# Optimization experiments

Hardware: AMD Instinct MI355X
Metric: run time of the kernel (lower is better)

The kernel has to match this reference:

```python
import jax, jax.numpy as jnp
import numpy as np

RES, RES_, STRIDE = 28, 14, 2
H, KD, AR = 8, 16, 4
SCALE = KD ** -0.5
EPS = 1e-5


def make_bias_idxs(res=RES, res_=RES_, stride=STRIDE):
    pts = [(i, j) for i in range(res) for j in range(res)]
    pts_ = [(i, j) for i in range(res_) for j in range(res_)]
    offs, idxs = {}, []
    for p1 in pts_:
        for p2 in pts:
            off = (abs(p1[0] * stride - p2[0]), abs(p1[1] * stride - p2[1]))
            if off not in offs:
                offs[off] = len(offs)
            idxs.append(offs[off])
    return np.array(idxs, dtype=np.int32).reshape(len(pts_), len(pts)), len(offs)


def setup_inputs() -> dict:
    key = jax.random.key(0)
    ks = jax.random.split(key, 16)
    idxs, n_off = make_bias_idxs()  # n_off == 784
    B, N, C = 128, RES * RES, 256
    d_kv, d_q, d_p, d_pin = 640, 128, 384, 512
    return {
        "hidden_state": jax.random.normal(ks[0], (B, N, C), jnp.float32),
        "w_kv": jax.random.normal(ks[1], (d_kv, C), jnp.float32) * 0.05,
        "kv_gamma": jax.random.uniform(ks[2], (d_kv,), jnp.float32, 0.5, 1.5),
        "kv_beta": jax.random.normal(ks[3], (d_kv,), jnp.float32) * 0.1,
        "kv_mean": jax.random.normal(ks[4], (d_kv,), jnp.float32) * 0.1,
        "kv_var": jax.random.uniform(ks[5], (d_kv,), jnp.float32, 0.5, 1.5),
        "w_q": jax.random.normal(ks[6], (d_q, C), jnp.float32) * 0.05,
        "q_gamma": jax.random.uniform(ks[7], (d_q,), jnp.float32, 0.5, 1.5),
        "q_beta": jax.random.normal(ks[8], (d_q,), jnp.float32) * 0.1,
        "q_mean": jax.random.normal(ks[9], (d_q,), jnp.float32) * 0.1,
        "q_var": jax.random.uniform(ks[10], (d_q,), jnp.float32, 0.5, 1.5),
        "w_proj": jax.random.normal(ks[11], (d_p, d_pin), jnp.float32) * 0.05,
        "p_gamma": jax.random.uniform(ks[12], (d_p,), jnp.float32, 0.5, 1.5),
        "p_beta": jax.random.normal(ks[13], (d_p,), jnp.float32) * 0.1,
        "p_mean": jax.random.normal(ks[14], (d_p,), jnp.float32) * 0.1,
        "p_var": jax.random.uniform(ks[15], (d_p,), jnp.float32, 0.5, 1.5),
        "attention_biases": jax.random.normal(jax.random.fold_in(key, 99), (H, n_off), jnp.float32),
        "attention_bias_idxs": jnp.asarray(idxs),
    }


def _bn(x, gamma, beta, mean, var):
    # eval-mode BatchNorm1d over last dim
    return (x - mean) * (gamma * jax.lax.rsqrt(var + EPS)) + beta


def _hardswish(x):
    return x * jnp.clip(x + 3.0, 0.0, 6.0) * (1.0 / 6.0)


def reference(hidden_state, w_kv, kv_gamma, kv_beta, kv_mean, kv_var,
              w_q, q_gamma, q_beta, q_mean, q_var,
              w_proj, p_gamma, p_beta, p_mean, p_var,
              attention_biases, attention_bias_idxs):
    B, N, C = hidden_state.shape
    N_ = RES_ * RES_
    # kv: [B, N, 640] -> key [B,H,N,KD], value [B,H,N,AR*KD]
    kv = _bn(hidden_state @ w_kv.T, kv_gamma, kv_beta, kv_mean, kv_var)
    kv = kv.reshape(B, N, H, KD + AR * KD)
    k = jnp.transpose(kv[..., :KD], (0, 2, 1, 3))          # [B,H,N,KD]
    v = jnp.transpose(kv[..., KD:], (0, 2, 1, 3))          # [B,H,N,AR*KD]
    # strided query subsample on the spatial grid
    hs = hidden_state.reshape(B, RES, RES, C)[:, ::STRIDE, ::STRIDE].reshape(B, N_, C)
    q = _bn(hs @ w_q.T, q_gamma, q_beta, q_mean, q_var)
    q = jnp.transpose(q.reshape(B, N_, H, KD), (0, 2, 1, 3))  # [B,H,N_,KD]
    bias = attention_biases[:, attention_bias_idxs]           # [H,N_,N] gathered
    attn = jnp.einsum('bhqd,bhkd->bhqk', q, k) * SCALE + bias
    attn = jax.nn.softmax(attn, axis=-1)
    out = jnp.einsum('bhqk,bhkd->bhqd', attn, v)              # [B,H,N_,AR*KD]
    out = jnp.transpose(out, (0, 2, 1, 3)).reshape(B, N_, H * AR * KD)
    out = _bn(_hardswish(out) @ w_proj.T, p_gamma, p_beta, p_mean, p_var)
    return out
```

## Files before the change

### kernel.cpp

```cpp
#include <hip/hip_runtime.h>

typedef _Float16 f16;
typedef __attribute__((ext_vector_type(2))) _Float16 f16x2;
typedef __attribute__((ext_vector_type(4))) _Float16 f16x4;
typedef __attribute__((ext_vector_type(8))) _Float16 f16x8;
typedef __attribute__((ext_vector_type(4))) float fvec4;
typedef __attribute__((ext_vector_type(4))) float f32x4;
typedef __attribute__((ext_vector_type(16))) float f32x16;
typedef __attribute__((ext_vector_type(4))) unsigned int uint4v;

#define NKEY 784
#define NKEYP 800
#define NQ 196
#define NQP 224

static __device__ __forceinline__ f32x4 mfma16(f16x8 a, f16x8 b, f32x4 c) {
    return __builtin_amdgcn_mfma_f32_16x16x32_f16(a, b, c, 0, 0, 0);
}
static __device__ __forceinline__ f32x16 mfma32(f16x8 a, f16x8 b, f32x16 c) {
    return __builtin_amdgcn_mfma_f32_32x32x16_f16(a, b, c, 0, 0, 0);
}
static __device__ __forceinline__ unsigned pk2(float a, float b) {
    f16x2 t; t[0] = (_Float16)a; t[1] = (_Float16)b;
    return __builtin_bit_cast(unsigned, t);
}
static __device__ __forceinline__ f32x16 z16() {
    f32x16 v;
#pragma unroll
    for (int i = 0; i < 16; ++i) v[i] = 0.f;
    return v;
}

__global__ void prep_scales_all(const float* __restrict__ kg, const float* __restrict__ kb,
                                const float* __restrict__ km, const float* __restrict__ kvv,
                                const float* __restrict__ qg, const float* __restrict__ qb,
                                const float* __restrict__ qm, const float* __restrict__ qv,
                                const float* __restrict__ pg, const float* __restrict__ pb,
                                const float* __restrict__ pm, const float* __restrict__ pv,
                                float* __restrict__ sb) {
    int i = blockIdx.x * 256 + threadIdx.x;
    if (i < 640) {
        float s = kg[i] * rsqrtf(kvv[i] + 1e-5f);
        sb[i] = s; sb[640 + i] = kb[i] - km[i] * s;
    } else if (i < 768) {
        int j = i - 640;
        float s = qg[j] * rsqrtf(qv[j] + 1e-5f);
        sb[1280 + j] = s; sb[1408 + j] = qb[j] - qm[j] * s;
    } else if (i < 1152) {
        int j = i - 768;
        float s = pg[j] * rsqrtf(pv[j] + 1e-5f);
        sb[1536 + j] = s; sb[1920 + j] = pb[j] - pm[j] * s;
    }
}

__global__ void conv_w(const float* __restrict__ wkv, const float* __restrict__ wq,
                       const float* __restrict__ wp, f16* __restrict__ out) {
    int i = blockIdx.x * 256 + threadIdx.x;
    const float* src;
    f16* dst;
    int kc, n, K;
    if (i < 20480)      { int j = i;         kc = j / 640, n = j - kc * 640; src = wkv; dst = out + (size_t)j * 8;            K = 256; }
    else if (i < 24576) { int j = i - 20480; kc = j / 128, n = j - kc * 128; src = wq;  dst = out + 163840 + (size_t)j * 8;   K = 256; }
    else                { int j = i - 24576; kc = j / 384, n = j - kc * 384; src = wp;  dst = out + 196608 + (size_t)j * 8;   K = 512; }
    const float* s = src + (size_t)n * K + kc * 8;
    fvec4 v0 = *(const fvec4*)s;
    fvec4 v1 = *(const fvec4*)(s + 4);
    f16x8 h;
    h[0] = (f16)v0[0]; h[1] = (f16)v0[1]; h[2] = (f16)v0[2]; h[3] = (f16)v0[3];
    h[4] = (f16)v1[0]; h[5] = (f16)v1[1]; h[6] = (f16)v1[2]; h[7] = (f16)v1[3];
    *(f16x8*)dst = h;
}

__global__ void prep_bias(const float* __restrict__ biases, const int* __restrict__ idxs,
                          f16* __restrict__ biasT, int n_off) {
    int tid = blockIdx.x * 256 + threadIdx.x;
    int h = tid / (NQP * NKEYP);
    int rem = tid - h * (NQP * NKEYP);
    int q = rem / NKEYP;
    int key = rem - q * NKEYP;
    float v = 0.f;
    if (q < NQ && key < NKEY) v = biases[h * n_off + idxs[q * NKEY + key]];
    biasT[tid] = (f16)v;
}

template <int MODE>
__global__ __launch_bounds__(256) void gemm_db(
        const void* __restrict__ Ap, const f16x8* __restrict__ Wg,
        const float* __restrict__ sc, const float* __restrict__ sh,
        void* __restrict__ OutA, f16* __restrict__ OutV) {
    constexpr int K     = (MODE == 2) ? 512 : 256;
    constexpr int KS    = K / 32;
    constexpr int CHUNK = (MODE == 2) ? 16 : 32;
    constexpr int NFR   = CHUNK / 16;
    constexpr int NT    = (MODE == 0) ? 640 : (MODE == 1 ? 128 : 384);
    constexpr int NCH   = (MODE == 0) ? 10 : (MODE == 1 ? 4 : 12);
    constexpr int UNITS = (K / 8) * CHUNK;
    constexpr int SR    = UNITS / 256;

    __shared__ f16x8 Wl[2][UNITS];

    const int t = threadIdx.x;
    const int lane = t & 63, wid = t >> 6;
    const int fr = lane & 15, kg = lane >> 4;
    const int m0 = blockIdx.x * 64;
    const int nb0 = blockIdx.y * (NCH * CHUNK);
    const int mrow = m0 + wid * 16 + fr;

    size_t arow;
    if constexpr (MODE == 1) {
        int b = mrow / 196, nn = mrow - b * 196;
        arow = (size_t)b * 784 + (nn / 14) * 56 + (nn % 14) * 2;
    } else {
        arow = (size_t)mrow;
    }
    f16x8 af[KS];
#pragma unroll
    for (int ks = 0; ks < KS; ++ks) {
        if constexpr (MODE == 2) {
            af[ks] = *(const f16x8*)((const f16*)Ap + arow * K + ks * 32 + kg * 8);
        } else {
            const float* a = (const float*)Ap + arow * 256 + ks * 32 + kg * 8;
            fvec4 v0 = *(const fvec4*)a;
            fvec4 v1 = *(const fvec4*)(a + 4);
            f16x8 hv;
            hv[0] = (f16)v0[0]; hv[1] = (f16)v0[1]; hv[2] = (f16)v0[2]; hv[3] = (f16)v0[3];
            hv[4] = (f16)v1[0]; hv[5] = (f16)v1[1]; hv[6] = (f16)v1[2]; hv[7] = (f16)v1[3];
            af[ks] = hv;
        }
    }

#pragma unroll
    for (int rr = 0; rr < SR; ++rr) {
        const int idx = rr * 256 + t;
        Wl[0][idx] = Wg[(size_t)(idx / CHUNK) * NT + nb0 + (idx % CHUNK)];
    }
    __syncthreads();

    const int rg = kg * 4;
    int cur = 0;
    for (int c = 0; c < NCH; ++c) {
        const int n0c = nb0 + c * CHUNK;

        f16x8 nx0, nx1, nx2, nx3;
        if (c + 1 < NCH) {
            const int n0n = n0c + CHUNK;
            nx0 = Wg[(size_t)((0 * 256 + t) / CHUNK) * NT + n0n + ((0 * 256 + t) % CHUNK)];
            nx1 = Wg[(size_t)((1 * 256 + t) / CHUNK) * NT + n0n + ((1 * 256 + t) % CHUNK)];
            nx2 = Wg[(size_t)((2 * 256 + t) / CHUNK) * NT + n0n + ((2 * 256 + t) % CHUNK)];
            nx3 = Wg[(size_t)((3 * 256 + t) / CHUNK) * NT + n0n + ((3 * 256 + t) % CHUNK)];
        }

        f32x4 acc[NFR];
#pragma unroll
        for (int j = 0; j < NFR; ++j) acc[j] = (f32x4){0.f, 0.f, 0.f, 0.f};
#pragma unroll
        for (int ks = 0; ks < KS; ++ks) {
            f16x8 bfr[NFR];
#pragma unroll
            for (int nf = 0; nf < NFR; ++nf)
                bfr[nf] = Wl[cur][(ks * 4 + kg) * CHUNK + nf * 16 + fr];
#pragma unroll
            for (int nf = 0; nf < NFR; ++nf)
                acc[nf] = mfma16(af[ks], bfr[nf], acc[nf]);
        }

        const int mbase = m0 + wid * 16 + rg;
#pragma unroll
        for (int nf = 0; nf < NFR; ++nf) {
            const int n = n0c + nf * 16 + fr;
            const float scn = sc[n], shn = sh[n];
            if constexpr (MODE == 0) {
                const int b = mbase / 784;
                const int nn = mbase - b * 784;
                const int hd = n / 80;
                const int cc = n - hd * 80;
                const size_t bh = (size_t)(b * 8 + hd);
                if (cc < 16) {
#pragma unroll
                    for (int r = 0; r < 4; ++r) {
                        float y = acc[nf][r] * scn + shn;
                        ((f16*)OutA)[(bh * NKEYP + nn + r) * 16 + cc] = (f16)y;
                    }
                } else {
                    const int kbk = nn >> 5, off = nn & 31;
                    f16x4 pv;
#pragma unroll
                    for (int r = 0; r < 4; ++r) pv[r] = (f16)(acc[nf][r] * scn + shn);
                    *(f16x4*)(OutV + ((bh * 25 + kbk) * 64 + (cc - 16)) * 32 + off) = pv;
                }
            } else if constexpr (MODE == 1) {
                const int b = mbase / 196;
                const int nn = mbase - b * 196;
                const int hd = n >> 4, cc = n & 15;
                const size_t bh = (size_t)(b * 8 + hd);
#pragma unroll
                for (int r = 0; r < 4; ++r) {
                    float y = acc[nf][r] * scn + shn;
                    ((f16*)OutA)[(bh * NQP + nn + r) * 16 + cc] = (f16)y;
                }
            } else {
#pragma unroll
                for (int r = 0; r < 4; ++r) {
                    float y = acc[nf][r] * scn + shn;
                    ((float*)OutA)[(size_t)(mbase + r) * 384 + n] = y;
                }
            }
        }

        if (c + 1 < NCH) {
            Wl[cur ^ 1][0 * 256 + t] = nx0;
            Wl[cur ^ 1][1 * 256 + t] = nx1;
            Wl[cur ^ 1][2 * 256 + t] = nx2;
            Wl[cur ^ 1][3 * 256 + t] = nx3;
            __syncthreads();
            cur ^= 1;
        }
    }
}

__global__ __launch_bounds__(448) void attn_fused(const f16* __restrict__ kb,
                                                  const f16* __restrict__ vtb,
                                                  const f16* __restrict__ qw,
                                                  const f16* __restrict__ biasT,
                                                  f16* __restrict__ ao) {
    const int bh = blockIdx.x;
    const int b = bh >> 3, h = bh & 7;
    const int wid = threadIdx.x >> 6;
    const int lane = threadIdx.x & 63;
    const int l31 = lane & 31;
    const int hh = lane >> 5;
    const int q0 = wid * 32;

    const f16* kp = kb + (size_t)bh * (NKEYP * 16);
    const f16* vp = vtb + (size_t)bh * (25 * 64 * 32) + l31 * 32;
    const f16x8 bq = *(const f16x8*)(qw + ((size_t)bh * NQP + q0 + l31) * 16 + hh * 8);
    const f16* bbq = biasT + ((size_t)h * NQP + (q0 + l31)) * NKEYP;

    float mrun = -1e30f;
    float lsum = 0.f;
    f32x16 o0 = z16(), o1 = z16();

    for (int key0 = 0; key0 < NKEY; key0 += 32) {
        f16x8 ak = *(const f16x8*)(kp + (size_t)(key0 + l31) * 16 + hh * 8);
        f32x16 s = mfma32(ak, bq, z16());
        const bool tail = (key0 + 32) > NKEY;
        f16x4 bw[4];
#pragma unroll
        for (int g = 0; g < 4; ++g)
            bw[g] = *(const f16x4*)(bbq + key0 + g * 8 + hh * 4);
        float p[16];
        float cmax = -3.0e38f;
#pragma unroll
        for (int r = 0; r < 16; ++r) {
            const int cr = (r & 3) + ((r >> 2) << 3) + (hh << 2);
            float sv = s[r] * 0.25f + (float)bw[r >> 2][r & 3];
            if (tail && (key0 + cr) >= NKEY) sv = -1e30f;
            p[r] = sv;
            cmax = fmaxf(cmax, sv);
        }
        cmax = fmaxf(cmax, __shfl_xor(cmax, 32));
        if (__any(cmax > mrun + 8.f)) {
            float mnew = fmaxf(mrun, cmax);
            float f = __expf(mrun - mnew);
            mrun = mnew;
            lsum *= f;
#pragma unroll
            for (int r = 0; r < 16; ++r) {
                const int cr = (r & 3) + ((r >> 2) << 3) + (hh << 2);
                float fr2 = __shfl(f, cr);
                o0[r] *= fr2;
                o1[r] *= fr2;
            }
        }
        float psum = 0.f;
#pragma unroll
        for (int r = 0; r < 16; ++r) {
            p[r] = __expf(p[r] - mrun);
            psum += p[r];
        }
        lsum += psum;
        unsigned g0l = pk2(p[0], p[1]),   g0h = pk2(p[2], p[3]);
        unsigned g1l = pk2(p[4], p[5]),   g1h = pk2(p[6], p[7]);
        unsigned g2l = pk2(p[8], p[9]),   g2h = pk2(p[10], p[11]);
        unsigned g3l = pk2(p[12], p[13]), g3h = pk2(p[14], p[15]);
        __builtin_amdgcn_s_setprio(1);
        const f16* vkb = vp + (key0 >> 5) * (64 * 32);
#pragma unroll
        for (int sH = 0; sH < 2; ++sH) {
            unsigned self_lo = sH ? (hh ? g3l : g2l) : (hh ? g1l : g0l);
            unsigned self_hi = sH ? (hh ? g3h : g2h) : (hh ? g1h : g0h);
            unsigned tx_lo   = sH ? (hh ? g2l : g3l) : (hh ? g0l : g1l);
            unsigned tx_hi   = sH ? (hh ? g2h : g3h) : (hh ? g0h : g1h);
            unsigned rx_lo = __shfl_xor(tx_lo, 32);
            unsigned rx_hi = __shfl_xor(tx_hi, 32);
            uint4v w;
            w[0] = hh ? rx_lo : self_lo;
            w[1] = hh ? rx_hi : self_hi;
            w[2] = hh ? self_lo : rx_lo;
            w[3] = hh ? self_hi : rx_hi;
            f16x8 pa = __builtin_bit_cast(f16x8, w);
            const f16* vrow = vkb + sH * 16 + hh * 8;
            f16x8 bv0 = *(const f16x8*)(vrow);
            f16x8 bv1 = *(const f16x8*)(vrow + 32 * 32);
            o0 = mfma32(pa, bv0, o0);
            o1 = mfma32(pa, bv1, o1);
        }
        __builtin_amdgcn_s_setprio(0);
    }
    lsum += __shfl_xor(lsum, 32);
    const float inv = 1.0f / lsum;
#pragma unroll
    for (int r = 0; r < 16; ++r) {
        const int cr = (r & 3) + ((r >> 2) << 3) + (hh << 2);
        const float iq = __shfl(inv, cr);
        const int qg = q0 + cr;
        if (qg < NQ) {
            float v0 = o0[r] * iq, v1 = o1[r] * iq;
            float h0 = v0 * fminf(fmaxf(v0 + 3.f, 0.f), 6.f) * (1.f / 6.f);
            float h1 = v1 * fminf(fmaxf(v1 + 3.f, 0.f), 6.f) * (1.f / 6.f);
            f16* dst = ao + ((size_t)b * NQ + qg) * 512 + h * 64 + l31;
            dst[0] = (f16)h0;
            dst[32] = (f16)h1;
        }
    }
}

extern "C" void kernel_launch(void* const* d_in, const int* in_sizes, int n_in,
                              void* d_out, int out_size, void* d_ws, size_t ws_size,
                              hipStream_t stream) {
    (void)n_in; (void)out_size; (void)ws_size;
    const float* hidden = (const float*)d_in[0];
    const float* w_kv   = (const float*)d_in[1];
    const float* w_q    = (const float*)d_in[6];
    const float* w_p    = (const float*)d_in[11];
    const float* biases = (const float*)d_in[16];
    const int*   idxs   = (const int*)d_in[17];
    const int n_off = in_sizes[16] / 8;

    char* ws = (char*)d_ws;
    const size_t OFF_K  = 0;
    const size_t OFF_V  = 26214400;
    const size_t OFF_Q  = 131072000;
    const size_t OFF_AO = 138412032;
    const size_t OFF_BT = 164102144;
    const size_t OFF_W  = 166969344;
    const size_t OFF_SC = 167755776;
    f16*   kbuf  = (f16*)(ws + OFF_K);
    f16*   vbuf  = (f16*)(ws + OFF_V);
    f16*   qbuf  = (f16*)(ws + OFF_Q);
    f16*   aobuf = (f16*)(ws + OFF_AO);
    f16*   btbuf = (f16*)(ws + OFF_BT);
    f16*   wf16  = (f16*)(ws + OFF_W);
    float* scbuf = (float*)(ws + OFF_SC);

    prep_scales_all<<<5, 256, 0, stream>>>(
        (const float*)d_in[2], (const float*)d_in[3], (const float*)d_in[4], (const float*)d_in[5],
        (const float*)d_in[7], (const float*)d_in[8], (const float*)d_in[9], (const float*)d_in[10],
        (const float*)d_in[12], (const float*)d_in[13], (const float*)d_in[14], (const float*)d_in[15],
        scbuf);
    conv_w<<<192, 256, 0, stream>>>(w_kv, w_q, w_p, wf16);
    prep_bias<<<5600, 256, 0, stream>>>(biases, idxs, btbuf, n_off);
    hipMemsetAsync(qbuf, 0, (size_t)1024 * NQP * 16 * 2, stream);
    gemm_db<0><<<dim3(1568, 2), 256, 0, stream>>>(hidden, (const f16x8*)wf16, scbuf, scbuf + 640, kbuf, vbuf);
    gemm_db<1><<<dim3(392, 1), 256, 0, stream>>>(hidden, (const f16x8*)(wf16 + 163840), scbuf + 1280, scbuf + 1408, qbuf, nullptr);
    attn_fused<<<1024, 448, 0, stream>>>(kbuf, vbuf, qbuf, btbuf, aobuf);
    gemm_db<2><<<dim3(392, 2), 256, 0, stream>>>(aobuf, (const f16x8*)(wf16 + 196608), scbuf + 1536, scbuf + 1920, d_out, nullptr);
}
```

Baseline: 226.6 us.

## Relayout bias and V tiles for coalesced MFMA-fragment loads, use exp2 softmax

The gathered bias table is now written in the exact per-lane MFMA accumulator order, so each lane fetches its 16 bias values with two contiguous 16-byte loads instead of four scattered 8-byte loads. The bias is pre-multiplied by log2(e) so the softmax can use exp2 with a folded scale. The V tile layout is split into 16-key halves so each lane's fragment read is a contiguous 16-byte row chunk. These changes target global-memory load efficiency in the attention inner loop, at the cost of more complex index arithmetic in the prep and GEMM-epilogue kernels.

```diff
diff --git a/kernel.cpp b/kernel.cpp
--- a/kernel.cpp
+++ b/kernel.cpp
@@ -13,6 +13,9 @@
 #define NKEYP 800
 #define NQ 196
 #define NQP 224
+#define LOG2E 1.442695041f
+#define SC2   0.360673760f
+#define THR2  11.5415603f
 
 static __device__ __forceinline__ f32x4 mfma16(f16x8 a, f16x8 b, f32x4 c) {
     return __builtin_amdgcn_mfma_f32_16x16x32_f16(a, b, c, 0, 0, 0);
@@ -72,15 +75,20 @@
 }
 
 __global__ void prep_bias(const float* __restrict__ biases, const int* __restrict__ idxs,
-                          f16* __restrict__ biasT, int n_off) {
+                          f16* __restrict__ biasS, int n_off) {
     int tid = blockIdx.x * 256 + threadIdx.x;
-    int h = tid / (NQP * NKEYP);
-    int rem = tid - h * (NQP * NKEYP);
-    int q = rem / NKEYP;
-    int key = rem - q * NKEYP;
+    const int r = tid & 15;
+    const int lane = (tid >> 4) & 63;
+    const int g = tid >> 10;
+    const int kbk = g % 25;
+    const int tmp = g / 25;
+    const int qt = tmp % 7;
+    const int h = tmp / 7;
+    const int q = qt * 32 + (lane & 31);
+    const int key = kbk * 32 + (r & 3) + 8 * (r >> 2) + 4 * (lane >> 5);
     float v = 0.f;
-    if (q < NQ && key < NKEY) v = biases[h * n_off + idxs[q * NKEY + key]];
-    biasT[tid] = (f16)v;
+    if (q < NQ && key < NKEY) v = biases[h * n_off + idxs[q * NKEY + key]] * LOG2E;
+    biasS[tid] = (f16)v;
 }
 
 template <int MODE>
@@ -182,11 +190,11 @@
                         ((f16*)OutA)[(bh * NKEYP + nn + r) * 16 + cc] = (f16)y;
                     }
                 } else {
-                    const int kbk = nn >> 5, off = nn & 31;
+                    const int kbk = nn >> 5, sH = (nn >> 4) & 1, kk = nn & 15;
                     f16x4 pv;
 #pragma unroll
                     for (int r = 0; r < 4; ++r) pv[r] = (f16)(acc[nf][r] * scn + shn);
-                    *(f16x4*)(OutV + ((bh * 25 + kbk) * 64 + (cc - 16)) * 32 + off) = pv;
+                    *(f16x4*)(OutV + ((bh * 25 + kbk) * 2 + sH) * 1024 + (cc - 16) * 16 + kk) = pv;
                 }
             } else if constexpr (MODE == 1) {
                 const int b = mbase / 196;
@@ -221,7 +229,7 @@
 __global__ __launch_bounds__(448) void attn_fused(const f16* __restrict__ kb,
                                                   const f16* __restrict__ vtb,
                                                   const f16* __restrict__ qw,
-                                                  const f16* __restrict__ biasT,
+                                                  const f16* __restrict__ biasS,
                                                   f16* __restrict__ ao) {
     const int bh = blockIdx.x;
     const int b = bh >> 3, h = bh & 7;
@@ -232,36 +240,36 @@
     const int q0 = wid * 32;
 
     const f16* kp = kb + (size_t)bh * (NKEYP * 16);
-    const f16* vp = vtb + (size_t)bh * (25 * 64 * 32) + l31 * 32;
+    const f16* vp = vtb + (size_t)bh * 51200;
     const f16x8 bq = *(const f16x8*)(qw + ((size_t)bh * NQP + q0 + l31) * 16 + hh * 8);
-    const f16* bbq = biasT + ((size_t)h * NQP + (q0 + l31)) * NKEYP;
+    const f16* bbase = biasS + (((size_t)(h * 7 + wid) * 25) * 64 + lane) * 16;
 
     float mrun = -1e30f;
     float lsum = 0.f;
     f32x16 o0 = z16(), o1 = z16();
 
     for (int key0 = 0; key0 < NKEY; key0 += 32) {
+        const int kbi = key0 >> 5;
         f16x8 ak = *(const f16x8*)(kp + (size_t)(key0 + l31) * 16 + hh * 8);
         f32x16 s = mfma32(ak, bq, z16());
         const bool tail = (key0 + 32) > NKEY;
-        f16x4 bw[4];
-#pragma unroll
-        for (int g = 0; g < 4; ++g)
-            bw[g] = *(const f16x4*)(bbq + key0 + g * 8 + hh * 4);
+        const f16x8* bp = (const f16x8*)(bbase + (size_t)kbi * 1024);
+        f16x8 b0 = bp[0], b1 = bp[1];
         float p[16];
         float cmax = -3.0e38f;
 #pragma unroll
         for (int r = 0; r < 16; ++r) {
             const int cr = (r & 3) + ((r >> 2) << 3) + (hh << 2);
-            float sv = s[r] * 0.25f + (float)bw[r >> 2][r & 3];
+            float bv = (r < 8) ? (float)b0[r] : (float)b1[r - 8];
+            float sv = s[r] * SC2 + bv;
             if (tail && (key0 + cr) >= NKEY) sv = -1e30f;
             p[r] = sv;
             cmax = fmaxf(cmax, sv);
         }
         cmax = fmaxf(cmax, __shfl_xor(cmax, 32));
-        if (__any(cmax > mrun + 8.f)) {
+        if (__any(cmax > mrun + THR2)) {
             float mnew = fmaxf(mrun, cmax);
-            float f = __expf(mrun - mnew);
+            float f = exp2f(mrun - mnew);
             mrun = mnew;
             lsum *= f;
 #pragma unroll
@@ -275,7 +283,7 @@
         float psum = 0.f;
 #pragma unroll
         for (int r = 0; r < 16; ++r) {
-            p[r] = __expf(p[r] - mrun);
+            p[r] = exp2f(p[r] - mrun);
             psum += p[r];
         }
         lsum += psum;
@@ -284,7 +292,7 @@
         unsigned g2l = pk2(p[8], p[9]),   g2h = pk2(p[10], p[11]);
         unsigned g3l = pk2(p[12], p[13]), g3h = pk2(p[14], p[15]);
         __builtin_amdgcn_s_setprio(1);
-        const f16* vkb = vp + (key0 >> 5) * (64 * 32);
+        const f16* vkb = vp + (size_t)kbi * 2048;
 #pragma unroll
         for (int sH = 0; sH < 2; ++sH) {
             unsigned self_lo = sH ? (hh ? g3l : g2l) : (hh ? g1l : g0l);
@@ -299,9 +307,9 @@
             w[2] = hh ? self_lo : rx_lo;
             w[3] = hh ? self_hi : rx_hi;
             f16x8 pa = __builtin_bit_cast(f16x8, w);
-            const f16* vrow = vkb + sH * 16 + hh * 8;
+            const f16* vrow = vkb + sH * 1024 + l31 * 16 + hh * 8;
             f16x8 bv0 = *(const f16x8*)(vrow);
-            f16x8 bv1 = *(const f16x8*)(vrow + 32 * 32);
+            f16x8 bv1 = *(const f16x8*)(vrow + 512);
             o0 = mfma32(pa, bv0, o0);
             o1 = mfma32(pa, bv1, o1);
         }
```

New measurement: 222.2 us. No clear change (-1.9%).
